# Optimization experiments

Hardware: AMD Instinct MI355X
Metric: run time of the kernel (lower is better)

Reference implementation:

```python
import jax, jax.numpy as jnp
import numpy as np

B, SEG, P, H, NH = 8, 16, 256, 1024, 16
DH = H // NH
T = P + 1                 # tokens per segment (segment lord + segment_size)
L = 1 + SEG * T           # 4113
LN_EPS = 1e-12


def setup_inputs() -> dict:
    key = jax.random.key(0)
    ks = jax.random.split(key, 9)
    s = 0.02
    return {
        "hidden_states": jax.random.normal(ks[0], (B, L, H), jnp.float32),
        "Blord_w": jax.random.normal(ks[1], (H, H), jnp.float32) * s,
        "Blord_b": jnp.zeros((H,), jnp.float32),
        "seg_qw": jax.random.normal(ks[2], (SEG, H, H), jnp.float32) * s,
        "seg_kw": jax.random.normal(ks[3], (SEG, H, H), jnp.float32) * s,
        "seg_vw": jax.random.normal(ks[4], (SEG, H, H), jnp.float32) * s,
        "lord_qw": jax.random.normal(ks[5], (H, H), jnp.float32) * s,
        "lord_kw": jax.random.normal(ks[6], (H, H), jnp.float32) * s,
        "lord_vw": jax.random.normal(ks[7], (H, H), jnp.float32) * s,
        "out_w": jax.random.normal(ks[8], (H, H), jnp.float32) * s,
        "out_b": jnp.zeros((H,), jnp.float32),
        "ln_w": jnp.ones((H,), jnp.float32),
        "ln_b": jnp.zeros((H,), jnp.float32),
    }


def reference(hidden_states, Blord_w, Blord_b, seg_qw, seg_kw, seg_vw,
              lord_qw, lord_kw, lord_vw, out_w, out_b, ln_w, ln_b):
    scale = 1.0 / np.sqrt(DH).astype(np.float32)

    # global lord projection of token 0 (torch Linear: x @ W.T + b)
    Blord = hidden_states[:, 0] @ Blord_w.T + Blord_b              # [B,H]

    # per-segment local full attention (each segment has its own QKV weights)
    seg_x = hidden_states[:, 1:].reshape(B, SEG, T, H)             # [B,S,T,H]
    q = jnp.einsum('bsti,soi->bsto', seg_x, seg_qw).reshape(B, SEG, T, NH, DH)
    k = jnp.einsum('bsti,soi->bsto', seg_x, seg_kw).reshape(B, SEG, T, NH, DH)
    v = jnp.einsum('bsti,soi->bsto', seg_x, seg_vw).reshape(B, SEG, T, NH, DH)
    scores = jnp.einsum('bsqhd,bskhd->bshqk', q, k) * scale        # [B,S,NH,T,T]
    probs = jax.nn.softmax(scores, axis=-1)
    seg_out = jnp.einsum('bshqk,bskhd->bsqhd', probs, v).reshape(B, SEG, T, H)

    # global attention over lord tokens: [Blord, seg_out[:, :, 0]]
    lords_in = jnp.concatenate([Blord[:, None, :], seg_out[:, :, 0, :]], axis=1)  # [B,S+1,H]
    lq = (lords_in @ lord_qw.T).reshape(B, SEG + 1, NH, DH)
    lk = (lords_in @ lord_kw.T).reshape(B, SEG + 1, NH, DH)
    lv = (lords_in @ lord_vw.T).reshape(B, SEG + 1, NH, DH)
    lscores = jnp.einsum('bqhd,bkhd->bhqk', lq, lk) * scale        # [B,NH,S+1,S+1]
    lprobs = jax.nn.softmax(lscores, axis=-1)
    lords = jnp.einsum('bhqk,bkhd->bqhd', lprobs, lv).reshape(B, SEG + 1, H)

    # reassemble: global lord, then per segment (updated lord token, local tokens)
    seg_out = seg_out.at[:, :, 0, :].set(lords[:, 1:])
    self_outputs = jnp.concatenate(
        [lords[:, :1], seg_out.reshape(B, SEG * T, H)], axis=1)    # [B,L,H]

    # output dense + residual + LayerNorm
    h = self_outputs @ out_w.T + out_b + hidden_states
    mu = h.mean(axis=-1, keepdims=True)
    var = h.var(axis=-1, keepdims=True)
    attention_output = (h - mu) / jnp.sqrt(var + LN_EPS) * ln_w + ln_b
    return attention_output, self_outputs
```

## Files before the change

### kernel.cpp

```cpp
#include <hip/hip_runtime.h>
#include <hip/hip_bf16.h>

typedef long long ll;
typedef __attribute__((ext_vector_type(8))) short bf16x8;
typedef __attribute__((ext_vector_type(4))) float fx4;

#define B_ 8
#define SEG_ 16
#define T_ 257
#define H_ 1024
#define NH_ 16
#define L_ 4113
#define SCALE 0.125f

__device__ __forceinline__ float bf2f(unsigned short u) {
  union { unsigned int i; float f; } w; w.i = ((unsigned int)u) << 16; return w.f;
}
__device__ __forceinline__ unsigned short f2bfu(float x) {
  __hip_bfloat16 h = __float2bfloat16(x);
  return *(unsigned short*)&h;
}

__device__ __forceinline__ void gl_lds16(const void* g, void* l) {
  __builtin_amdgcn_global_load_lds((const __attribute__((address_space(1))) void*)g,
                                   (__attribute__((address_space(3))) void*)l, 16, 0, 0);
}

#define NU_HID 4211712
#define NU_W   2097152
#define NU_OW  131072
__global__ __launch_bounds__(256) void f2bf_all(
    const float* __restrict__ hid, __hip_bfloat16* __restrict__ hbf,
    const float* __restrict__ wq, const float* __restrict__ wk, const float* __restrict__ wv,
    __hip_bfloat16* __restrict__ w3,
    const float* __restrict__ ow, __hip_bfloat16* __restrict__ owb)
{
  const int NTOT = NU_HID + 3 * NU_W + NU_OW;
  for (int i = blockIdx.x * 256 + threadIdx.x; i < NTOT; i += gridDim.x * 256) {
    const float* src;
    __hip_bfloat16* dst;
    if (i < NU_HID) {
      src = hid + (ll)i * 8;
      dst = hbf + (ll)i * 8;
    } else if (i < NU_HID + 3 * NU_W) {
      int j = i - NU_HID;
      int which = j >> 21;
      int off = j & (NU_W - 1);
      const float* ws = (which == 0) ? wq : (which == 1) ? wk : wv;
      src = ws + (ll)off * 8;
      dst = w3 + (ll)j * 8;
    } else {
      int k = i - NU_HID - 3 * NU_W;
      src = ow + (ll)k * 8;
      dst = owb + (ll)k * 8;
    }
    float4 a = ((const float4*)src)[0];
    float4 b = ((const float4*)src)[1];
    union { bf16x8 v; unsigned short u[8]; } o;
    o.u[0] = f2bfu(a.x); o.u[1] = f2bfu(a.y); o.u[2] = f2bfu(a.z); o.u[3] = f2bfu(a.w);
    o.u[4] = f2bfu(b.x); o.u[5] = f2bfu(b.y); o.u[6] = f2bfu(b.z); o.u[7] = f2bfu(b.w);
    *(bf16x8*)dst = o.v;
  }
}

__global__ __launch_bounds__(256) void gemm_qkv(
    const __hip_bfloat16* __restrict__ A,
    const __hip_bfloat16* __restrict__ Wall,
    __hip_bfloat16* __restrict__ Cq,
    __hip_bfloat16* __restrict__ Ck,
    __hip_bfloat16* __restrict__ Cv)
{
  const int nwg = 24 * 17 * 16;
  const int orig = blockIdx.x + 24 * (blockIdx.y + 17 * blockIdx.z);
  const int swz = (orig & 7) * (nwg >> 3) + (orig >> 3);
  const int by = swz % 17;
  const int tt = swz / 17;
  const int bx = tt % 24;
  const int bz = tt / 24;
  const int which = bx >> 3;
  const int n0 = (bx & 7) * 128;
  const int m0 = by * 128;
  const int M = B_ * T_;

  const __hip_bfloat16* W = Wall + ((ll)which * SEG_ + bz) * ((ll)H_ * H_);
  __hip_bfloat16* C = (which == 0) ? Cq : (which == 1) ? Ck : Cv;

  __shared__ __hip_bfloat16 At[3][128 * 32];
  __shared__ __hip_bfloat16 Bt[3][128 * 32];

  const int tid = threadIdx.x;
  const int lane = tid & 63;
  const int wid = tid >> 6;
  const int wm = (wid >> 1) * 64;
  const int wn = (wid & 1) * 64;

  const int r0 = tid >> 2;
  const int p = tid & 3;
  const int kc  = p * 8;
  const int kcs = (p ^ ((r0 >> 1) & 3)) * 8;
  const int am0 = min(m0 + r0, M - 1);
  const int am1 = min(m0 + 64 + r0, M - 1);
  const ll segoff = (ll)bz * ((ll)T_ * H_);
  const ll aoff0 = (ll)(am0 / T_) * ((ll)L_ * H_) + segoff + (ll)(am0 % T_) * H_;
  const ll aoff1 = (ll)(am1 / T_) * ((ll)L_ * H_) + segoff + (ll)(am1 % T_) * H_;
  const ll boff0 = (ll)(n0 + r0) * H_;
  const ll boff1 = (ll)(n0 + 64 + r0) * H_;
  const int stA0 = r0 * 32 + kc;

  fx4 acc[4][4];
#pragma unroll
  for (int i = 0; i < 4; ++i)
#pragma unroll
    for (int j = 0; j < 4; ++j) acc[i][j] = fx4{0.f, 0.f, 0.f, 0.f};

  const int sw = ((lane & 15) >> 1) & 3;
  const int fragA = (wm + (lane & 15)) * 32 + (((lane >> 4) ^ sw) << 3);
  const int fragB = (wn + (lane & 15)) * 32 + (((lane >> 4) ^ sw) << 3);

#define STAGE_QKV(buf, kt) do { const int kk = (kt) * 32; \
    gl_lds16(A + aoff0 + kk + kcs, (void*)(&At[buf][0] + stA0)); \
    gl_lds16(A + aoff1 + kk + kcs, (void*)(&At[buf][0] + 2048 + stA0)); \
    gl_lds16(W + boff0 + kk + kcs, (void*)(&Bt[buf][0] + stA0)); \
    gl_lds16(W + boff1 + kk + kcs, (void*)(&Bt[buf][0] + 2048 + stA0)); } while (0)

  STAGE_QKV(0, 0);
  STAGE_QKV(1, 1);
  for (int t = 0; t < 32; ++t) {
    __builtin_amdgcn_s_barrier();
    asm volatile("" ::: "memory");
    if (t + 2 < 32) { const int b3 = (t + 2) % 3; STAGE_QKV(b3, t + 2); }
    if (t < 30)       asm volatile("s_waitcnt vmcnt(8)" ::: "memory");
    else if (t == 30) asm volatile("s_waitcnt vmcnt(4)" ::: "memory");
    else              asm volatile("s_waitcnt vmcnt(0)" ::: "memory");
    __builtin_amdgcn_s_barrier();
    asm volatile("" ::: "memory");

    const int cb = t % 3;
    const __hip_bfloat16* ap = &At[cb][0] + fragA;
    const __hip_bfloat16* bp = &Bt[cb][0] + fragB;
    bf16x8 af[4], bfr[4];
#pragma unroll
    for (int f = 0; f < 4; ++f) {
      af[f]  = *(const bf16x8*)(ap + f * 16 * 32);
      bfr[f] = *(const bf16x8*)(bp + f * 16 * 32);
    }
    __builtin_amdgcn_s_setprio(1);
#pragma unroll
    for (int mf = 0; mf < 4; ++mf)
#pragma unroll
      for (int nf = 0; nf < 4; ++nf)
        acc[mf][nf] = __builtin_amdgcn_mfma_f32_16x16x32_bf16(af[mf], bfr[nf], acc[mf][nf], 0, 0, 0);
    __builtin_amdgcn_s_setprio(0);
  }
#undef STAGE_QKV

  const int cn = n0 + wn + (lane & 15);
#pragma unroll
  for (int mf = 0; mf < 4; ++mf) {
    int mloc = m0 + wm + mf * 16 + ((lane >> 4) << 2);
#pragma unroll
    for (int r = 0; r < 4; ++r) {
      int m = mloc + r;
      if (m >= M) continue;
      ll co = ((ll)(m / T_) * SEG_ + bz) * ((ll)T_ * H_) + (ll)(m % T_) * H_;
#pragma unroll
      for (int nf = 0; nf < 4; ++nf)
        C[co + cn + nf * 16] = __float2bfloat16(acc[mf][nf][r]);
    }
  }
}

__global__ __launch_bounds__(256) void gemm_out(
    const __hip_bfloat16* __restrict__ A,
    const __hip_bfloat16* __restrict__ W,
    const float* __restrict__ bias,
    float* __restrict__ C,
    const float* __restrict__ res)
{
  const int nwg = 8 * 258;
  const int orig = blockIdx.x + 8 * blockIdx.y;
  const int swz = (orig & 7) * (nwg >> 3) + (orig >> 3);
  const int bx = swz % 8;
  const int by = swz / 8;
  const int M = B_ * L_;
  const int m0 = by * 128;
  const int n0 = bx * 128;

  __shared__ __hip_bfloat16 At[3][128 * 32];
  __shared__ __hip_bfloat16 Bt[3][128 * 32];

  const int tid = threadIdx.x;
  const int lane = tid & 63;
  const int wid = tid >> 6;
  const int wm = (wid >> 1) * 64;
  const int wn = (wid & 1) * 64;

  const int r0 = tid >> 2;
  const int p = tid & 3;
  const int kc  = p * 8;
  const int kcs = (p ^ ((r0 >> 1) & 3)) * 8;
  const ll aoff0 = (ll)min(m0 + r0, M - 1) * H_;
  const ll aoff1 = (ll)min(m0 + 64 + r0, M - 1) * H_;
  const ll boff0 = (ll)(n0 + r0) * H_;
  const ll boff1 = (ll)(n0 + 64 + r0) * H_;
  const int stA0 = r0 * 32 + kc;

  fx4 acc[4][4];
#pragma unroll
  for (int i = 0; i < 4; ++i)
#pragma unroll
    for (int j = 0; j < 4; ++j) acc[i][j] = fx4{0.f, 0.f, 0.f, 0.f};

  const int sw = ((lane & 15) >> 1) & 3;
  const int fragA = (wm + (lane & 15)) * 32 + (((lane >> 4) ^ sw) << 3);
  const int fragB = (wn + (lane & 15)) * 32 + (((lane >> 4) ^ sw) << 3);

#define STAGE_O(buf, kt) do { const int kk = (kt) * 32; \
    gl_lds16(A + aoff0 + kk + kcs, (void*)(&At[buf][0] + stA0)); \
    gl_lds16(A + aoff1 + kk + kcs, (void*)(&At[buf][0] + 2048 + stA0)); \
    gl_lds16(W + boff0 + kk + kcs, (void*)(&Bt[buf][0] + stA0)); \
    gl_lds16(W + boff1 + kk + kcs, (void*)(&Bt[buf][0] + 2048 + stA0)); } while (0)

  STAGE_O(0, 0);
  STAGE_O(1, 1);
  for (int t = 0; t < 32; ++t) {
    __builtin_amdgcn_s_barrier();
    asm volatile("" ::: "memory");
    if (t + 2 < 32) { const int b3 = (t + 2) % 3; STAGE_O(b3, t + 2); }
    if (t < 30)       asm volatile("s_waitcnt vmcnt(8)" ::: "memory");
    else if (t == 30) asm volatile("s_waitcnt vmcnt(4)" ::: "memory");
    else              asm volatile("s_waitcnt vmcnt(0)" ::: "memory");
    __builtin_amdgcn_s_barrier();
    asm volatile("" ::: "memory");

    const int cb = t % 3;
    const __hip_bfloat16* ap = &At[cb][0] + fragA;
    const __hip_bfloat16* bp = &Bt[cb][0] + fragB;
    bf16x8 af[4], bfr[4];
#pragma unroll
    for (int f = 0; f < 4; ++f) {
      af[f]  = *(const bf16x8*)(ap + f * 16 * 32);
      bfr[f] = *(const bf16x8*)(bp + f * 16 * 32);
    }
    __builtin_amdgcn_s_setprio(1);
#pragma unroll
    for (int mf = 0; mf < 4; ++mf)
#pragma unroll
      for (int nf = 0; nf < 4; ++nf)
        acc[mf][nf] = __builtin_amdgcn_mfma_f32_16x16x32_bf16(af[mf], bfr[nf], acc[mf][nf], 0, 0, 0);
    __builtin_amdgcn_s_setprio(0);
  }
#undef STAGE_O

  const int cn = n0 + wn + (lane & 15);
#pragma unroll
  for (int mf = 0; mf < 4; ++mf) {
    int mloc = m0 + wm + mf * 16 + ((lane >> 4) << 2);
#pragma unroll
    for (int r = 0; r < 4; ++r) {
      int m = mloc + r;
      if (m >= M) continue;
#pragma unroll
      for (int nf = 0; nf < 4; ++nf) {
        int n = cn + nf * 16;
        C[(ll)m * H_ + n] = acc[mf][nf][r] + bias[n] + res[(ll)m * H_ + n];
      }
    }
  }
}

__global__ __launch_bounds__(256) void seg_attn_mfma(
    const __hip_bfloat16* __restrict__ Qb,
    const __hip_bfloat16* __restrict__ Kb,
    const __hip_bfloat16* __restrict__ Vb,
    float* __restrict__ so, __hip_bfloat16* __restrict__ sob)
{
  __shared__ __align__(16) char smem[8192 + 9216 + 4 * 4096];
  char* KsB = smem;
  char* VTB = smem + 8192;
  const int tid = threadIdx.x, lane = tid & 63, wid = tid >> 6;
  char* PB = smem + 8192 + 9216 + wid * 4096;

  const int h = blockIdx.y, bs = blockIdx.z;
  const int b = bs >> 4, s = bs & 15;
  const int q0 = blockIdx.x * 128 + wid * 32;
  const ll base = (ll)bs * (T_ * H_) + h * 64;

  bf16x8 qf[2][2];
#pragma unroll
  for (int mf = 0; mf < 2; ++mf) {
    int qr = q0 + mf * 16 + (lane & 15);
#pragma unroll
    for (int ks = 0; ks < 2; ++ks)
      qf[mf][ks] = *(const bf16x8*)(Qb + base + (ll)qr * H_ + ks * 32 + ((lane >> 4) << 3));
  }

  float l_[2][4];
  fx4 of[2][4];
#pragma unroll
  for (int mf = 0; mf < 2; ++mf) {
#pragma unroll
    for (int r = 0; r < 4; ++r) l_[mf][r] = 0.f;
#pragma unroll
    for (int df = 0; df < 4; ++df) of[mf][df] = fx4{0.f, 0.f, 0.f, 0.f};
  }

  const int krow = tid >> 3;
  const int kc8 = tid & 7;
  const int kkp = tid & 31;
  const int vd0 = (tid >> 5) * 8;

  for (int t = 0; t < 5; ++t) {
    const int k0 = t * 64;
    __syncthreads();
    {
      int row = krow;
      int kr = k0 + row; if (kr > 256) kr = 256;
      gl_lds16(Kb + base + (ll)kr * H_ + ((kc8 ^ (row & 7)) << 3), KsB + tid * 16);
      row = krow + 32;
      kr = k0 + row; if (kr > 256) kr = 256;
      gl_lds16(Kb + base + (ll)kr * H_ + ((kc8 ^ (row & 7)) << 3), KsB + 4096 + tid * 16);
    }
    {
      int kk = kkp * 2;
      int kr0 = k0 + kk;     if (kr0 > 256) kr0 = 256;
      int kr1 = k0 + kk + 1; if (kr1 > 256) kr1 = 256;
      bf16x8 v0 = *(const bf16x8*)(Vb + base + (ll)kr0 * H_ + vd0);
      bf16x8 v1 = *(const bf16x8*)(Vb + base + (ll)kr1 * H_ + vd0);
      unsigned int* vtu = (unsigned int*)VTB;
#pragma unroll
      for (int j = 0; j < 8; ++j)
        vtu[(vd0 + j) * 36 + kkp] =
            (unsigned int)(unsigned short)v0[j] | ((unsigned int)(unsigned short)v1[j] << 16);
    }
    __syncthreads();

    {
      fx4 sa[2][4];
#pragma unroll
      for (int mf = 0; mf < 2; ++mf)
#pragma unroll
        for (int nf = 0; nf < 4; ++nf) sa[mf][nf] = fx4{0.f, 0.f, 0.f, 0.f};
#pragma unroll
      for (int nf = 0; nf < 4; ++nf) {
        int key = nf * 16 + (lane & 15);
#pragma unroll
        for (int ks = 0; ks < 2; ++ks) {
          int c16 = ks * 4 + (lane >> 4);
          bf16x8 kf = *(const bf16x8*)(KsB + key * 128 + ((c16 ^ (key & 7)) << 4));
          sa[0][nf] = __builtin_amdgcn_mfma_f32_16x16x32_bf16(qf[0][ks], kf, sa[0][nf], 0, 0, 0);
          sa[1][nf] = __builtin_amdgcn_mfma_f32_16x16x32_bf16(qf[1][ks], kf, sa[1][nf], 0, 0, 0);
        }
      }
#pragma unroll
      for (int nf = 0; nf < 4; ++nf) {
        bool bad = (k0 + nf * 16 + (lane & 15)) > 256;
#pragma unroll
        for (int mf = 0; mf < 2; ++mf) {
#pragma unroll
          for (int r = 0; r < 4; ++r) {
            float pexp = bad ? 0.f : __expf(sa[mf][nf][r] * SCALE);
            sa[mf][nf][r] = pexp;
            l_[mf][r] += pexp;
          }
        }
      }
#pragma unroll
      for (int mf = 0; mf < 2; ++mf)
#pragma unroll
        for (int nf = 0; nf < 4; ++nf)
#pragma unroll
          for (int rp = 0; rp < 2; ++rp) {
            float v0 = sa[mf][nf][rp];
            float v2 = sa[mf][nf][rp + 2];
            float o0 = __shfl_xor(v0, 1);
            float o2 = __shfl_xor(v2, 1);
            const bool odd = (lane & 1);
            float lo = odd ? o2 : v0;
            float hi = odd ? v2 : o0;
            unsigned int pk = (unsigned int)f2bfu(lo) | ((unsigned int)f2bfu(hi) << 16);
            int row = mf * 16 + ((lane >> 4) << 2) + (odd ? rp + 2 : rp);
            int col2 = nf * 16 + (lane & 14);
            *(unsigned int*)(PB + row * 128 + ((col2 * 2) ^ ((row & 7) << 4))) = pk;
          }
#pragma unroll
      for (int kks = 0; kks < 2; ++kks) {
        bf16x8 pa[2];
#pragma unroll
        for (int mf = 0; mf < 2; ++mf) {
          int prow = mf * 16 + (lane & 15);
          int c16 = kks * 4 + (lane >> 4);
          pa[mf] = *(const bf16x8*)(PB + prow * 128 + ((c16 ^ (prow & 7)) << 4));
        }
#pragma unroll
        for (int df = 0; df < 4; ++df) {
          bf16x8 vf = *(const bf16x8*)(VTB + (df * 16 + (lane & 15)) * 144 + kks * 64 + ((lane >> 4) << 4));
          of[0][df] = __builtin_amdgcn_mfma_f32_16x16x32_bf16(pa[0], vf, of[0][df], 0, 0, 0);
          of[1][df] = __builtin_amdgcn_mfma_f32_16x16x32_bf16(pa[1], vf, of[1][df], 0, 0, 0);
        }
      }
    }
  }

  {
#pragma unroll
    for (int mf = 0; mf < 2; ++mf)
#pragma unroll
      for (int r = 0; r < 4; ++r) {
        float rs = l_[mf][r];
        rs += __shfl_xor(rs, 1);
        rs += __shfl_xor(rs, 2);
        rs += __shfl_xor(rs, 4);
        rs += __shfl_xor(rs, 8);
        l_[mf][r] = rs;
      }
#pragma unroll
    for (int mf = 0; mf < 2; ++mf)
#pragma unroll
      for (int r = 0; r < 4; ++r) {
        int q = q0 + mf * 16 + ((lane >> 4) << 2) + r;
        float inv = 1.f / l_[mf][r];
        ll rowoff = ((ll)b * L_ + 1 + (ll)s * T_ + q) * H_ + h * 64;
#pragma unroll
        for (int df = 0; df < 4; ++df) {
          int d = df * 16 + (lane & 15);
          float v = of[mf][df][r] * inv;
          so[rowoff + d] = v;
          sob[rowoff + d] = __float2bfloat16(v);
        }
      }
  }
}

__global__ __launch_bounds__(64) void seg_attn_tail(
    const __hip_bfloat16* __restrict__ Qb,
    const __hip_bfloat16* __restrict__ Kb,
    const __hip_bfloat16* __restrict__ Vb,
    float* __restrict__ so, __hip_bfloat16* __restrict__ sob)
{
  const int h = blockIdx.x & 15;
  const int bs = blockIdx.x >> 4;
  const int b = bs >> 4, s = bs & 15;
  const int lane = threadIdx.x;
  const ll base = (ll)bs * (T_ * H_) + h * 64;

  __shared__ float qs[64];
  __shared__ float osum[64][65];

  if (lane < 8) {
    bf16x8 qv = *(const bf16x8*)(Qb + base + (ll)256 * H_ + lane * 8);
#pragma unroll
    for (int j = 0; j < 8; ++j) qs[lane * 8 + j] = bf2f((unsigned short)qv[j]);
  }
  __syncthreads();

  float l_part = 0.f;
  float o[64];
#pragma unroll
  for (int d = 0; d < 64; ++d) o[d] = 0.f;

  const int nk = (lane == 0) ? 5 : 4;
  for (int kk = 0; kk < nk; ++kk) {
    int key = (kk == 4) ? 256 : kk * 64 + lane;
    const __hip_bfloat16* kp = Kb + base + (ll)key * H_;
    const __hip_bfloat16* vp = Vb + base + (ll)key * H_;
    float sc = 0.f;
    float vv[64];
#pragma unroll
    for (int c = 0; c < 8; ++c) {
      bf16x8 kv8 = *(const bf16x8*)(kp + c * 8);
      bf16x8 vv8 = *(const bf16x8*)(vp + c * 8);
#pragma unroll
      for (int j = 0; j < 8; ++j) {
        sc = fmaf(qs[c * 8 + j], bf2f((unsigned short)kv8[j]), sc);
        vv[c * 8 + j] = bf2f((unsigned short)vv8[j]);
      }
    }
    float pe = __expf(sc * SCALE);
    l_part += pe;
#pragma unroll
    for (int d = 0; d < 64; ++d) o[d] = fmaf(pe, vv[d], o[d]);
  }

  float l = l_part;
  l += __shfl_xor(l, 1);  l += __shfl_xor(l, 2);  l += __shfl_xor(l, 4);
  l += __shfl_xor(l, 8);  l += __shfl_xor(l, 16); l += __shfl_xor(l, 32);

#pragma unroll
  for (int d = 0; d < 64; ++d) osum[lane][d] = o[d];
  __syncthreads();
  float od = 0.f;
#pragma unroll
  for (int r = 0; r < 64; ++r) od += osum[r][lane];
  od /= l;
  ll rowoff = ((ll)b * L_ + 1 + (ll)s * T_ + 256) * H_ + h * 64 + lane;
  so[rowoff] = od;
  sob[rowoff] = __float2bfloat16(od);
}

__global__ __launch_bounds__(256) void gemm_bt(
    const float* __restrict__ X, ll xbs,
    const float* __restrict__ W,
    const float* __restrict__ bias,
    float* __restrict__ C, ll cbs,
    int M, int K)
{
  const int tid = threadIdx.x;
  const int n0 = blockIdx.x * 64;

  __shared__ float Xt[16][68];
  __shared__ float Wt[16][68];

  const int lr = tid >> 2;
  const int lc = (tid & 3) << 2;
  const int mload = min(lr, M - 1);
  const ll xoff = (ll)mload * xbs;
  const ll woff = (ll)(n0 + lr) * K;

  const int tr = tid >> 4;
  const int tc = tid & 15;

  float acc[4][4];
#pragma unroll
  for (int i = 0; i < 4; ++i)
#pragma unroll
    for (int j = 0; j < 4; ++j) acc[i][j] = 0.f;

  for (int k0 = 0; k0 < K; k0 += 16) {
    float4 xv = *(const float4*)(X + xoff + k0 + lc);
    float4 wv = *(const float4*)(W + woff + k0 + lc);
    __syncthreads();
    Xt[lc + 0][lr] = xv.x; Xt[lc + 1][lr] = xv.y; Xt[lc + 2][lr] = xv.z; Xt[lc + 3][lr] = xv.w;
    Wt[lc + 0][lr] = wv.x; Wt[lc + 1][lr] = wv.y; Wt[lc + 2][lr] = wv.z; Wt[lc + 3][lr] = wv.w;
    __syncthreads();
#pragma unroll
    for (int kk = 0; kk < 16; ++kk) {
      float4 xa = *(const float4*)&Xt[kk][tr << 2];
      float4 wb = *(const float4*)&Wt[kk][tc << 2];
      float xa_[4] = {xa.x, xa.y, xa.z, xa.w};
      float wb_[4] = {wb.x, wb.y, wb.z, wb.w};
#pragma unroll
      for (int i = 0; i < 4; ++i)
#pragma unroll
        for (int j = 0; j < 4; ++j)
          acc[i][j] = fmaf(xa_[i], wb_[j], acc[i][j]);
    }
  }

#pragma unroll
  for (int i = 0; i < 4; ++i) {
    int m = (tr << 2) + i;
    if (m >= M) continue;
#pragma unroll
    for (int j = 0; j < 4; ++j) {
      int n = n0 + (tc << 2) + j;
      C[(ll)m * cbs + n] = acc[i][j] + (bias ? bias[n] : 0.f);
    }
  }
}

__global__ __launch_bounds__(256) void lord_proj(
    const float* __restrict__ blord,
    const float* __restrict__ so,
    const float* __restrict__ Wq, const float* __restrict__ Wk, const float* __restrict__ Wv,
    float* __restrict__ Cq, float* __restrict__ Ck, float* __restrict__ Cv)
{
  const float* W = (blockIdx.z == 0) ? Wq : (blockIdx.z == 1) ? Wk : Wv;
  float* C = (blockIdx.z == 0) ? Cq : (blockIdx.z == 1) ? Ck : Cv;
  const int M = 136, K = 1024;

  const int tid = threadIdx.x;
  const int m0 = blockIdx.y * 64;
  const int n0 = blockIdx.x * 64;

  __shared__ float Xt[16][68];
  __shared__ float Wt[16][68];

  const int lr = tid >> 2;
  const int lc = (tid & 3) << 2;
  const int mload = min(m0 + lr, M - 1);
  const int bb = mload / 17, rr = mload % 17;
  const float* xrow = (rr == 0)
      ? (blord + (ll)mload * 1024)
      : (so + ((ll)bb * L_ + 1 + (ll)(rr - 1) * T_) * H_);
  const ll woff = (ll)(n0 + lr) * K;

  const int tr = tid >> 4;
  const int tc = tid & 15;

  float acc[4][4];
#pragma unroll
  for (int i = 0; i < 4; ++i)
#pragma unroll
    for (int j = 0; j < 4; ++j) acc[i][j] = 0.f;

  for (int k0 = 0; k0 < K; k0 += 16) {
    float4 xv = *(const float4*)(xrow + k0 + lc);
    float4 wv = *(const float4*)(W + woff + k0 + lc);
    __syncthreads();
    Xt[lc + 0][lr] = xv.x; Xt[lc + 1][lr] = xv.y; Xt[lc + 2][lr] = xv.z; Xt[lc + 3][lr] = xv.w;
    Wt[lc + 0][lr] = wv.x; Wt[lc + 1][lr] = wv.y; Wt[lc + 2][lr] = wv.z; Wt[lc + 3][lr] = wv.w;
    __syncthreads();
#pragma unroll
    for (int kk = 0; kk < 16; ++kk) {
      float4 xa = *(const float4*)&Xt[kk][tr << 2];
      float4 wb = *(const float4*)&Wt[kk][tc << 2];
      float xa_[4] = {xa.x, xa.y, xa.z, xa.w};
      float wb_[4] = {wb.x, wb.y, wb.z, wb.w};
#pragma unroll
      for (int i = 0; i < 4; ++i)
#pragma unroll
        for (int j = 0; j < 4; ++j)
          acc[i][j] = fmaf(xa_[i], wb_[j], acc[i][j]);
    }
  }

#pragma unroll
  for (int i = 0; i < 4; ++i) {
    int m = m0 + (tr << 2) + i;
    if (m >= M) continue;
#pragma unroll
    for (int j = 0; j < 4; ++j)
      C[(ll)m * 1024 + n0 + (tc << 2) + j] = acc[i][j];
  }
}

__global__ __launch_bounds__(256) void lord_attn2(
    const float* __restrict__ lq, const float* __restrict__ lk,
    const float* __restrict__ lv, float* __restrict__ so,
    __hip_bfloat16* __restrict__ sob)
{
  const int b = blockIdx.x, h = blockIdx.y;
  const int tid = threadIdx.x, lane = tid & 63, wid = tid >> 6;
  __shared__ float Qs[17][64], Ks[17][64], Vs[17][64];
  for (int t = tid; t < 17 * 64; t += 256) {
    int r = t >> 6, c = t & 63;
    ll g = ((ll)(b * 17 + r)) * H_ + h * 64 + c;
    Qs[r][c] = lq[g];
    Ks[r][c] = lk[g];
    Vs[r][c] = lv[g];
  }
  __syncthreads();
  for (int q = wid; q < 17; q += 4) {
    float qd = Qs[q][lane];
    float sc[17];
#pragma unroll
    for (int k = 0; k < 17; ++k) {
      float p = qd * Ks[k][lane];
      p += __shfl_xor(p, 1);  p += __shfl_xor(p, 2);  p += __shfl_xor(p, 4);
      p += __shfl_xor(p, 8);  p += __shfl_xor(p, 16); p += __shfl_xor(p, 32);
      sc[k] = p * SCALE;
    }
    float mx = sc[0];
#pragma unroll
    for (int k = 1; k < 17; ++k) mx = fmaxf(mx, sc[k]);
    float l = 0.f;
#pragma unroll
    for (int k = 0; k < 17; ++k) { sc[k] = __expf(sc[k] - mx); l += sc[k]; }
    float invl = 1.f / l;
    float o = 0.f;
#pragma unroll
    for (int k = 0; k < 17; ++k) o = fmaf(sc[k], Vs[k][lane], o);
    o *= invl;
    ll row = (q == 0) ? (ll)b * L_ : ((ll)b * L_ + 1 + (ll)(q - 1) * T_);
    so[row * H_ + h * 64 + lane] = o;
    sob[row * H_ + h * 64 + lane] = __float2bfloat16(o);
  }
}

__global__ __launch_bounds__(256) void ln_inplace(
    float* __restrict__ hbuf, const float* __restrict__ w, const float* __restrict__ bgain)
{
  const ll row = blockIdx.x;
  const int tid = threadIdx.x;
  float4 x = *(float4*)(hbuf + row * H_ + tid * 4);
  float s = x.x + x.y + x.z + x.w;
  float s2 = x.x * x.x + x.y * x.y + x.z * x.z + x.w * x.w;
#pragma unroll
  for (int off = 32; off >= 1; off >>= 1) {
    s  += __shfl_down(s, off, 64);
    s2 += __shfl_down(s2, off, 64);
  }
  __shared__ float red[2][4];
  int wid = tid >> 6;
  if ((tid & 63) == 0) { red[0][wid] = s; red[1][wid] = s2; }
  __syncthreads();
  s  = red[0][0] + red[0][1] + red[0][2] + red[0][3];
  s2 = red[1][0] + red[1][1] + red[1][2] + red[1][3];
  const float mean = s * (1.f / H_);
  float var = s2 * (1.f / H_) - mean * mean;
  var = fmaxf(var, 0.f);
  const float inv = rsqrtf(var + 1e-12f);
  float4 g = *(const float4*)(w + tid * 4);
  float4 bb = *(const float4*)(bgain + tid * 4);
  float4 y;
  y.x = (x.x - mean) * inv * g.x + bb.x;
  y.y = (x.y - mean) * inv * g.y + bb.y;
  y.z = (x.z - mean) * inv * g.z + bb.z;
  y.w = (x.w - mean) * inv * g.w + bb.w;
  *(float4*)(hbuf + row * H_ + tid * 4) = y;
}

extern "C" void kernel_launch(void* const* d_in, const int* in_sizes, int n_in,
                              void* d_out, int out_size, void* d_ws, size_t ws_size,
                              hipStream_t stream)
{
  const float* hidden  = (const float*)d_in[0];
  const float* Blord_w = (const float*)d_in[1];
  const float* Blord_b = (const float*)d_in[2];
  const float* seg_qw  = (const float*)d_in[3];
  const float* seg_kw  = (const float*)d_in[4];
  const float* seg_vw  = (const float*)d_in[5];
  const float* lord_qw = (const float*)d_in[6];
  const float* lord_kw = (const float*)d_in[7];
  const float* lord_vw = (const float*)d_in[8];
  const float* out_w   = (const float*)d_in[9];
  const float* out_b   = (const float*)d_in[10];
  const float* ln_w    = (const float*)d_in[11];
  const float* ln_b    = (const float*)d_in[12];

  float* attn_out = (float*)d_out;
  float* self_out = (float*)d_out + (ll)B_ * L_ * H_;

  const ll QKV = (ll)B_ * SEG_ * T_ * H_;
  const ll SHH = (ll)SEG_ * H_ * H_;
  __hip_bfloat16* qb = (__hip_bfloat16*)attn_out;
  __hip_bfloat16* kb = qb + QKV;
  __hip_bfloat16* hbf = (__hip_bfloat16*)self_out;
  __hip_bfloat16* vb = (__hip_bfloat16*)d_ws;
  __hip_bfloat16* wslot3 = vb + QKV;
  __hip_bfloat16* sob = wslot3;
  __hip_bfloat16* outw_bf = wslot3 + 3 * SHH;
  float* lords_in = (float*)(outw_bf + (ll)H_ * H_);
  float* lqw_ = lords_in + 136 * 1024;
  float* lkw_ = lqw_ + 136 * 1024;
  float* lvw_ = lkw_ + 136 * 1024;

  dim3 blk(256);

  f2bf_all<<<dim3(2048), blk, 0, stream>>>(
      hidden, hbf, seg_qw, seg_kw, seg_vw, wslot3, out_w, outw_bf);

  gemm_qkv<<<dim3(24, 17, 16), blk, 0, stream>>>(hbf + H_, wslot3, qb, kb, vb);

  gemm_bt<<<dim3(16), blk, 0, stream>>>(
      hidden, (ll)L_ * H_, Blord_w, Blord_b, lords_in, (ll)17 * H_, B_, H_);

  seg_attn_mfma<<<dim3(2, NH_, B_ * SEG_), blk, 0, stream>>>(qb, kb, vb, self_out, sob);
  seg_attn_tail<<<dim3(B_ * SEG_ * NH_), dim3(64), 0, stream>>>(qb, kb, vb, self_out, sob);

  lord_proj<<<dim3(16, 3, 3), blk, 0, stream>>>(
      lords_in, self_out, lord_qw, lord_kw, lord_vw, lqw_, lkw_, lvw_);

  lord_attn2<<<dim3(B_, NH_), blk, 0, stream>>>(lqw_, lkw_, lvw_, self_out, sob);

  gemm_out<<<dim3(8, 258), blk, 0, stream>>>(sob, outw_bf, out_b, attn_out, hidden);

  ln_inplace<<<dim3(B_ * L_), blk, 0, stream>>>(attn_out, ln_w, ln_b);
}
```

Before: 855.4 us.

## Double-buffer K and V tiles in segment attention to overlap loads with MFMA

The segment attention kernel now keeps two LDS buffers each for K and transposed V. The next tile's K is prefetched with global_load_lds and its V is loaded into registers while the current tile is computed, and the V transpose write plus a single barrier happen after the compute. This hides global load latency and drops one barrier per iteration. The cost is more LDS per block (about 51KB instead of 34KB), which may lower occupancy, and more live registers.

```diff
diff --git a/kernel.cpp b/kernel.cpp
--- a/kernel.cpp
+++ b/kernel.cpp
@@ -275,11 +275,11 @@
     const __hip_bfloat16* __restrict__ Vb,
     float* __restrict__ so, __hip_bfloat16* __restrict__ sob)
 {
-  __shared__ __align__(16) char smem[8192 + 9216 + 4 * 4096];
-  char* KsB = smem;
-  char* VTB = smem + 8192;
+  __shared__ __align__(16) char smem[2 * 8192 + 2 * 9216 + 4 * 4096];
+  char* Ks0 = smem;
+  char* VT0 = smem + 16384;
   const int tid = threadIdx.x, lane = tid & 63, wid = tid >> 6;
-  char* PB = smem + 8192 + 9216 + wid * 4096;
+  char* PB = smem + 16384 + 18432 + wid * 4096;
 
   const int h = blockIdx.y, bs = blockIdx.z;
   const int b = bs >> 4, s = bs & 15;
@@ -310,32 +310,51 @@
   const int kkp = tid & 31;
   const int vd0 = (tid >> 5) * 8;
 
+#define STAGE_K(koff, k0_) do { \
+    int row = krow; \
+    int kr = (k0_) + row; if (kr > 256) kr = 256; \
+    gl_lds16(Kb + base + (ll)kr * H_ + ((kc8 ^ (row & 7)) << 3), Ks0 + (koff) + tid * 16); \
+    row = krow + 32; \
+    kr = (k0_) + row; if (kr > 256) kr = 256; \
+    gl_lds16(Kb + base + (ll)kr * H_ + ((kc8 ^ (row & 7)) << 3), Ks0 + (koff) + 4096 + tid * 16); \
+  } while (0)
+
+#define WRITE_VT(voff, v0_, v1_) do { \
+    unsigned int* vtu = (unsigned int*)(VT0 + (voff)); \
+    _Pragma("unroll") \
+    for (int j = 0; j < 8; ++j) \
+      vtu[(vd0 + j) * 36 + kkp] = \
+          (unsigned int)(unsigned short)(v0_)[j] | ((unsigned int)(unsigned short)(v1_)[j] << 16); \
+  } while (0)
+
+  {
+    STAGE_K(0, 0);
+    int kk = kkp * 2;
+    int kr0 = min(kk, 256), kr1 = min(kk + 1, 256);
+    bf16x8 v0 = *(const bf16x8*)(Vb + base + (ll)kr0 * H_ + vd0);
+    bf16x8 v1 = *(const bf16x8*)(Vb + base + (ll)kr1 * H_ + vd0);
+    asm volatile("s_waitcnt vmcnt(0)" ::: "memory");
+    WRITE_VT(0, v0, v1);
+    __syncthreads();
+  }
+
+  int kco = 0, vto = 0;
   for (int t = 0; t < 5; ++t) {
     const int k0 = t * 64;
-    __syncthreads();
+    const bool pre = (t + 1 < 5);
+    bf16x8 v0r, v1r;
+    if (pre) {
+      const int kn = k0 + 64;
+      STAGE_K(kco ^ 8192, kn);
+      int kk = kkp * 2;
+      int kr0 = min(kn + kk, 256), kr1 = min(kn + kk + 1, 256);
+      v0r = *(const bf16x8*)(Vb + base + (ll)kr0 * H_ + vd0);
+      v1r = *(const bf16x8*)(Vb + base + (ll)kr1 * H_ + vd0);
+    }
+
     {
-      int row = krow;
-      int kr = k0 + row; if (kr > 256) kr = 256;
-      gl_lds16(Kb + base + (ll)kr * H_ + ((kc8 ^ (row & 7)) << 3), KsB + tid * 16);
-      row = krow + 32;
-      kr = k0 + row; if (kr > 256) kr = 256;
-      gl_lds16(Kb + base + (ll)kr * H_ + ((kc8 ^ (row & 7)) << 3), KsB + 4096 + tid * 16);
-    }
-    {
-      int kk = kkp * 2;
-      int kr0 = k0 + kk;     if (kr0 > 256) kr0 = 256;
-      int kr1 = k0 + kk + 1; if (kr1 > 256) kr1 = 256;
-      bf16x8 v0 = *(const bf16x8*)(Vb + base + (ll)kr0 * H_ + vd0);
-      bf16x8 v1 = *(const bf16x8*)(Vb + base + (ll)kr1 * H_ + vd0);
-      unsigned int* vtu = (unsigned int*)VTB;
-#pragma unroll
-      for (int j = 0; j < 8; ++j)
-        vtu[(vd0 + j) * 36 + kkp] =
-            (unsigned int)(unsigned short)v0[j] | ((unsigned int)(unsigned short)v1[j] << 16);
-    }
-    __syncthreads();
-
-    {
+      const char* KsB = Ks0 + kco;
+      const char* VTB = VT0 + vto;
       fx4 sa[2][4];
 #pragma unroll
       for (int mf = 0; mf < 2; ++mf)
@@ -400,7 +419,16 @@
         }
       }
     }
-  }
+
+    if (pre) {
+      asm volatile("s_waitcnt vmcnt(0)" ::: "memory");
+      WRITE_VT(vto ^ 9216, v0r, v1r);
+      __syncthreads();
+      kco ^= 8192; vto ^= 9216;
+    }
+  }
+#undef STAGE_K
+#undef WRITE_VT
 
   {
 #pragma unroll
```

Result: slower. 874.8 us (+2.3%).
